# Optimization experiments

Measured on AMD Instinct MI355X. Metric: run time of the kernel, lower is better.

## Reference

```python
import jax, jax.numpy as jnp
import numpy as np

N = 50000
E = 800000
FEAT = 128
COND = 64
HID = 128
LAT = 64


def setup_inputs() -> dict:
    key = jax.random.key(0)
    ks = jax.random.split(key, 16)
    inp = {
        "feature": jax.random.normal(ks[0], (N, FEAT), jnp.float32),
        "condition": jax.random.normal(ks[1], (N, COND), jnp.float32),
        "edge_index": jax.random.randint(ks[2], (2, E), 0, N, jnp.int64 if jax.config.jax_enable_x64 else jnp.int32),
        "noise": jax.random.normal(ks[3], (N, LAT), jnp.float32),
        # GCNConv params (glorot-style scale)
        "W_f2h": jax.random.normal(ks[4], (FEAT, HID), jnp.float32) * (1.0 / np.sqrt(FEAT)),
        "b_f2h": jnp.zeros((HID,), jnp.float32),
        "W_c2h": jax.random.normal(ks[5], (COND, HID), jnp.float32) * (1.0 / np.sqrt(COND)),
        "b_c2h": jnp.zeros((HID,), jnp.float32),
        "W_h2h": jax.random.normal(ks[6], (2 * HID, HID), jnp.float32) * (1.0 / np.sqrt(2 * HID)),
        "b_h2h": jnp.zeros((HID,), jnp.float32),
        "W_mean": jax.random.normal(ks[7], (HID, LAT), jnp.float32) * (1.0 / np.sqrt(HID)),
        "b_mean": jnp.zeros((LAT,), jnp.float32),
        "W_logvar": jax.random.normal(ks[8], (HID, LAT), jnp.float32) * (1.0 / np.sqrt(HID)),
        "b_logvar": jnp.zeros((LAT,), jnp.float32),
    }
    return inp


def _gcn_norm(edge_index, n):
    # add self-loops, compute symmetric normalization deg^-1/2 * deg^-1/2
    loop = jnp.arange(n, dtype=edge_index.dtype)
    src = jnp.concatenate([edge_index[0], loop])
    dst = jnp.concatenate([edge_index[1], loop])
    deg = jax.ops.segment_sum(jnp.ones_like(src, jnp.float32), dst, num_segments=n)
    dinv = jnp.where(deg > 0, jax.lax.rsqrt(deg), 0.0)
    norm = dinv[src] * dinv[dst]  # [E+N]
    return src, dst, norm


def _gcn_conv(x, W, b, src, dst, norm, n):
    h = x @ W                                  # [N, out]
    msg = h[src] * norm[:, None]               # gather + scale, [E+N, out]
    out = jax.ops.segment_sum(msg, dst, num_segments=n)
    return out + b


def reference(feature, condition, edge_index, noise,
              W_f2h, b_f2h, W_c2h, b_c2h, W_h2h, b_h2h,
              W_mean, b_mean, W_logvar, b_logvar):
    n = feature.shape[0]
    src, dst, norm = _gcn_norm(edge_index, n)
    f2h = jnp.tanh(_gcn_conv(feature, W_f2h, b_f2h, src, dst, norm, n))
    c2h = jnp.tanh(_gcn_conv(condition, W_c2h, b_c2h, src, dst, norm, n))
    h = jnp.concatenate([f2h, c2h], axis=1)
    h = jnp.tanh(_gcn_conv(h, W_h2h, b_h2h, src, dst, norm, n))
    mean = _gcn_conv(h, W_mean, b_mean, src, dst, norm, n)
    logvar = _gcn_conv(h, W_logvar, b_logvar, src, dst, norm, n)
    z = noise * jnp.exp(0.5 * logvar) + mean
    return (z, mean, logvar)
```

## Files before the change

### kernel.cpp

```cpp
#include <hip/hip_runtime.h>
#include <math.h>

namespace {

constexpr int N = 50000;
constexpr int E = 800000;

typedef __attribute__((ext_vector_type(8))) short short8;
typedef __attribute__((ext_vector_type(4))) float f32x4;
typedef __attribute__((ext_vector_type(2))) float f32x2;


__device__ inline unsigned short f2bf(float f) {
  unsigned int b = __float_as_uint(f);
  unsigned int r = (b + 0x7fffu + ((b >> 16) & 1u)) >> 16;
  return (unsigned short)r;
}
__device__ inline unsigned int pack2(float a, float b) {
  return (unsigned int)f2bf(a) | ((unsigned int)f2bf(b) << 16);
}


__device__ inline unsigned int pack4_fp8(float a, float b, float c, float d) {
  int w = 0;
  w = __builtin_amdgcn_cvt_pk_fp8_f32(a, b, w, false);
  w = __builtin_amdgcn_cvt_pk_fp8_f32(c, d, w, true);
  return (unsigned int)w;
}
__device__ inline unsigned char f2fp8(float v) {
  return (unsigned char)(__builtin_amdgcn_cvt_pk_fp8_f32(v, v, 0, false) & 0xff);
}


__global__ void zero_int(int* p, int n) {
  int i = blockIdx.x * blockDim.x + threadIdx.x;
  if (i < n) p[i] = 0;
}

__global__ __launch_bounds__(256) void count_xcd(const int* __restrict__ dst,
                                                 int* __restrict__ cnt) {
  constexpr int RANGE = (N + 7) / 8;
  int r = blockIdx.x & 7;
  int lo = r * RANGE;
  int hi = lo + RANGE;
  int nb = gridDim.x >> 3;
  int bi = blockIdx.x >> 3;
  for (int e = bi * 256 + threadIdx.x; e < E; e += nb * 256) {
    int d = dst[e];
    if (d >= lo && d < hi) atomicAdd(&cnt[d], 1);
  }
}

__global__ void block_sums(const int* __restrict__ cnt, int* __restrict__ bsum, int n) {
  int tid = threadIdx.x;
  int i = blockIdx.x * 256 + tid;
  int v = (i < n) ? cnt[i] : 0;
  for (int off = 32; off > 0; off >>= 1) v += __shfl_down(v, off, 64);
  __shared__ int sred[4];
  if ((tid & 63) == 0) sred[tid >> 6] = v;
  __syncthreads();
  if (tid == 0) bsum[blockIdx.x] = sred[0] + sred[1] + sred[2] + sred[3];
}

__global__ void scan_chunks2(const int* __restrict__ cnt, const int* __restrict__ bsum,
                             int nbk, int* __restrict__ row_ptr, int* __restrict__ cursor,
                             float* __restrict__ dinv, int n) {
  __shared__ int s[256];
  __shared__ int sred[4];
  __shared__ int sprefix;
  int tid = threadIdx.x;
  int pv = (tid < nbk && tid < (int)blockIdx.x) ? bsum[tid] : 0;
  for (int off = 32; off > 0; off >>= 1) pv += __shfl_down(pv, off, 64);
  if ((tid & 63) == 0) sred[tid >> 6] = pv;
  __syncthreads();
  if (tid == 0) sprefix = sred[0] + sred[1] + sred[2] + sred[3];
  int i = blockIdx.x * 256 + tid;
  int v = (i < n) ? cnt[i] : 0;
  s[tid] = v;
  __syncthreads();
  for (int d = 1; d < 256; d <<= 1) {
    int t = (tid >= d) ? s[tid - d] : 0;
    __syncthreads();
    s[tid] += t;
    __syncthreads();
  }
  if (i < n) {
    int excl = sprefix + s[tid] - v;
    row_ptr[i] = excl;
    cursor[i] = excl;
    dinv[i] = rsqrtf((float)(v + 1));
    if (i == n - 1) row_ptr[n] = excl + v;
  }
}

__global__ __launch_bounds__(256) void scatter_xcd(const int* __restrict__ src,
                                                   const int* __restrict__ dst,
                                                   int* __restrict__ cursor,
                                                   int* __restrict__ csr_src) {
  constexpr int RANGE = (N + 7) / 8;
  int r = blockIdx.x & 7;
  int lo = r * RANGE;
  int hi = lo + RANGE;
  int nb = gridDim.x >> 3;
  int bi = blockIdx.x >> 3;
  for (int e = bi * 256 + threadIdx.x; e < E; e += nb * 256) {
    int d = dst[e];
    if (d >= lo && d < hi) {
      int pos = atomicAdd(&cursor[d], 1);
      csr_src[pos] = src[e];
    }
  }
}


__global__ void cvt_cond(const float* __restrict__ in, const float* __restrict__ dinv,
                         unsigned char* __restrict__ out, int n) {
  int t = blockIdx.x * blockDim.x + threadIdx.x;
  if (t >= n * 8) return;
  int i = t >> 3, j = t & 7;
  float di = dinv[i];
  const float* s = in + (size_t)i * 64 + j * 8;
  float4 a = *(const float4*)s;
  float4 b = *(const float4*)(s + 4);
  uint2 o;
  o.x = pack4_fp8(di * a.x, di * a.y, di * a.z, di * a.w);
  o.y = pack4_fp8(di * b.x, di * b.y, di * b.z, di * b.w);
  *(uint2*)(out + (size_t)i * 192 + 128 + j * 8) = o;
}

__global__ void pack_w(const float* __restrict__ W1, int s1,
                       const float* __restrict__ W2, int s2, int split,
                       int ksteps, unsigned short* __restrict__ out) {
  int t = blockIdx.x * blockDim.x + threadIdx.x;
  int total = ksteps * 8 * 64;
  if (t >= total) return;
  int ks = t >> 9;
  int ct = (t >> 6) & 7;
  int l = t & 63;
  int k0 = ks * 32 + ((l >> 4) << 3);
  int col = ct * 16 + (l & 15);
  const float* src;
  int c;
  if (col < split) { src = W1 + col; c = s1; }
  else { src = W2 + (col - split); c = s2; }
  unsigned short* o = out + (size_t)t * 8;
#pragma unroll
  for (int i = 0; i < 8; ++i) o[i] = f2bf(src[(size_t)(k0 + i) * c]);
}

__global__ void make_bcat(const float* __restrict__ bm, const float* __restrict__ bl,
                          float* __restrict__ bcat) {
  int j = threadIdx.x;
  if (j < 64) bcat[j] = bm[j];
  else if (j < 128) bcat[j] = bl[j - 64];
}


template <int K, int EPI, bool F32A, int OUT>
__global__ __launch_bounds__(256) void gemm_mfma(const void* __restrict__ Av, int lda,
                                                 const unsigned short* __restrict__ Wp,
                                                 const float* __restrict__ bias_or_scale,
                                                 void* __restrict__ Cv, int ldc, int n) {
  constexpr int KSTEPS = K / 32;
  int tid = threadIdx.x;
  int w = tid >> 6;
  int l = tid & 63;
  int r0 = blockIdx.x * 128 + w * 32;
  int arow = l & 15;
  int kgrp = l >> 4;

  f32x4 acc[2][8];
#pragma unroll
  for (int m = 0; m < 2; ++m)
#pragma unroll
    for (int ct = 0; ct < 8; ++ct) acc[m][ct] = (f32x4)(0.f);

  int ra0 = min(r0 + arow, n - 1);
  int ra1 = min(r0 + 16 + arow, n - 1);

#pragma unroll 1
  for (int ks = 0; ks < KSTEPS; ++ks) {
    short8 a0, a1;
    if (F32A) {
      const float* p0 = (const float*)Av + (size_t)ra0 * lda + kgrp * 8 + ks * 32;
      const float* p1 = (const float*)Av + (size_t)ra1 * lda + kgrp * 8 + ks * 32;
      float4 x0 = *(const float4*)p0, y0 = *(const float4*)(p0 + 4);
      float4 x1 = *(const float4*)p1, y1 = *(const float4*)(p1 + 4);
      unsigned int u[4];
      u[0] = pack2(x0.x, x0.y); u[1] = pack2(x0.z, x0.w);
      u[2] = pack2(y0.x, y0.y); u[3] = pack2(y0.z, y0.w);
      a0 = *(const short8*)u;
      u[0] = pack2(x1.x, x1.y); u[1] = pack2(x1.z, x1.w);
      u[2] = pack2(y1.x, y1.y); u[3] = pack2(y1.z, y1.w);
      a1 = *(const short8*)u;
    } else {
      a0 = *(const short8*)((const unsigned short*)Av + (size_t)ra0 * lda + kgrp * 8 + ks * 32);
      a1 = *(const short8*)((const unsigned short*)Av + (size_t)ra1 * lda + kgrp * 8 + ks * 32);
    }
    const short8* pb = (const short8*)Wp + (size_t)(ks * 8) * 64 + l;
#pragma unroll
    for (int ct = 0; ct < 8; ++ct) {
      short8 b = pb[ct * 64];
      acc[0][ct] = __builtin_amdgcn_mfma_f32_16x16x32_bf16(a0, b, acc[0][ct], 0, 0, 0);
      acc[1][ct] = __builtin_amdgcn_mfma_f32_16x16x32_bf16(a1, b, acc[1][ct], 0, 0, 0);
    }
  }

  int ccol = l & 15;
  int crow = (l >> 4) * 4;
#pragma unroll
  for (int ct = 0; ct < 8; ++ct) {
    int col = ct * 16 + ccol;
    float bv = (EPI == 1) ? bias_or_scale[col] : 0.f;
#pragma unroll
    for (int m = 0; m < 2; ++m) {
#pragma unroll
      for (int r = 0; r < 4; ++r) {
        int row = r0 + m * 16 + crow + r;
        if (row < n) {
          float v = acc[m][ct][r];
          if (EPI == 1) v = tanhf(v + bv);
          if (EPI == 2) v = v * bias_or_scale[row];
          if (OUT == 0)
            ((unsigned short*)Cv)[(size_t)row * ldc + col] = f2bf(v);
          else
            ((unsigned char*)Cv)[(size_t)row * ldc + col] = f2fp8(v);
        }
      }
    }
  }
}


#define ACC16_ADD_FP8(ACC, U)                                           \
  {                                                                     \
    f32x2 t0 = __builtin_amdgcn_cvt_pk_f32_fp8((int)U.x, false);        \
    f32x2 t1 = __builtin_amdgcn_cvt_pk_f32_fp8((int)U.x, true);         \
    f32x2 t2 = __builtin_amdgcn_cvt_pk_f32_fp8((int)U.y, false);        \
    f32x2 t3 = __builtin_amdgcn_cvt_pk_f32_fp8((int)U.y, true);         \
    f32x2 t4 = __builtin_amdgcn_cvt_pk_f32_fp8((int)U.z, false);        \
    f32x2 t5 = __builtin_amdgcn_cvt_pk_f32_fp8((int)U.z, true);         \
    f32x2 t6 = __builtin_amdgcn_cvt_pk_f32_fp8((int)U.w, false);        \
    f32x2 t7 = __builtin_amdgcn_cvt_pk_f32_fp8((int)U.w, true);         \
    ACC[0] += t0[0]; ACC[1] += t0[1]; ACC[2] += t1[0]; ACC[3] += t1[1]; \
    ACC[4] += t2[0]; ACC[5] += t2[1]; ACC[6] += t3[0]; ACC[7] += t3[1]; \
    ACC[8] += t4[0]; ACC[9] += t4[1]; ACC[10] += t5[0]; ACC[11] += t5[1]; \
    ACC[12] += t6[0]; ACC[13] += t6[1]; ACC[14] += t7[0]; ACC[15] += t7[1]; \
  }

#define EDGE_WALK_PIPE(LANES, ROWSTRIDE)                                \
  int deg = e1 - e0;                                                    \
  int idxA = csr_src[e0 + wl];                                          \
  int idxB = csr_src[e0 + LANES + wl];                                  \
  int cnext = e0 + 2 * LANES;                                           \
  int t = 0;                                                            \
  while (t < deg) {                                                     \
    int idxN = csr_src[cnext + wl];                                     \
    _Pragma("unroll")                                                   \
    for (int k = 0; k < LANES; ++k) {                                   \
      if (t + k < deg) {                                                \
        int s = __shfl(idxA, rowbase + k);                              \
        uint4 u = X16[(size_t)s * ROWSTRIDE + wl];                      \
        ACC16_ADD_FP8(acc, u)                                           \
      }                                                                 \
    }                                                                   \
    idxA = idxB; idxB = idxN;                                           \
    cnext += LANES; t += LANES;                                         \
  }


__global__ __launch_bounds__(256) void prop192(const unsigned char* __restrict__ X,
                                               unsigned short* __restrict__ f2h_out,
                                               unsigned short* __restrict__ pc_out,
                                               const int* __restrict__ row_ptr,
                                               const int* __restrict__ csr_src,
                                               const float* __restrict__ dinv,
                                               const float* __restrict__ b_f2h, int n) {
  int wave = threadIdx.x >> 6;
  int wlane = threadIdx.x & 63;
  int rrow = wlane / 12;
  int wl = wlane - rrow * 12;
  if (rrow >= 5) return;
  int rowbase = rrow * 12;
  int i = blockIdx.x * 20 + wave * 5 + rrow;
  if (i >= n) return;
  const uint4* X16 = (const uint4*)X;
  float di = dinv[i];
  float acc[16];
#pragma unroll
  for (int j = 0; j < 16; ++j) acc[j] = 0.f;
  {
    uint4 u = X16[(size_t)i * 12 + wl];
    ACC16_ADD_FP8(acc, u)
  }
  int e0 = row_ptr[i], e1 = row_ptr[i + 1];
  EDGE_WALK_PIPE(12, 12)

  if (wl < 8) {
    float out[16];
#pragma unroll
    for (int j = 0; j < 16; ++j) out[j] = tanhf(fmaf(di, acc[j], b_f2h[wl * 16 + j]));
    unsigned short* yp = f2h_out + (size_t)i * 256 + wl * 16;
    uint4 o0, o1;
    o0.x = pack2(out[0], out[1]); o0.y = pack2(out[2], out[3]);
    o0.z = pack2(out[4], out[5]); o0.w = pack2(out[6], out[7]);
    o1.x = pack2(out[8], out[9]); o1.y = pack2(out[10], out[11]);
    o1.z = pack2(out[12], out[13]); o1.w = pack2(out[14], out[15]);
    *(uint4*)yp = o0;
    *(uint4*)(yp + 8) = o1;
  } else {
    unsigned short* yp = pc_out + (size_t)i * 64 + (wl - 8) * 16;
    uint4 o0, o1;
    o0.x = pack2(di * acc[0], di * acc[1]); o0.y = pack2(di * acc[2], di * acc[3]);
    o0.z = pack2(di * acc[4], di * acc[5]); o0.w = pack2(di * acc[6], di * acc[7]);
    o1.x = pack2(di * acc[8], di * acc[9]); o1.y = pack2(di * acc[10], di * acc[11]);
    o1.z = pack2(di * acc[12], di * acc[13]); o1.w = pack2(di * acc[14], di * acc[15]);
    *(uint4*)yp = o0;
    *(uint4*)(yp + 8) = o1;
  }
}


__global__ __launch_bounds__(256) void prop128(const unsigned char* __restrict__ X,
                                               unsigned short* __restrict__ Y,
                                               const int* __restrict__ row_ptr,
                                               const int* __restrict__ csr_src,
                                               const float* __restrict__ dinv,
                                               const float* __restrict__ bias, int n) {
  int wl = threadIdx.x & 7;
  int rloc = threadIdx.x >> 3;
  int rowbase = (threadIdx.x & 63) & ~7;
  int i = blockIdx.x * 32 + rloc;
  if (i >= n) return;
  const uint4* X16 = (const uint4*)X;
  float di = dinv[i];
  float acc[16];
#pragma unroll
  for (int j = 0; j < 16; ++j) acc[j] = 0.f;
  {
    uint4 u = X16[(size_t)i * 8 + wl];
    ACC16_ADD_FP8(acc, u)
  }
  int e0 = row_ptr[i], e1 = row_ptr[i + 1];
  EDGE_WALK_PIPE(8, 8)

  float out[16];
#pragma unroll
  for (int j = 0; j < 16; ++j) out[j] = tanhf(fmaf(di, acc[j], bias[wl * 16 + j]));
  unsigned short* yp = Y + (size_t)i * 128 + wl * 16;
  uint4 o0, o1;
  o0.x = pack2(out[0], out[1]); o0.y = pack2(out[2], out[3]);
  o0.z = pack2(out[4], out[5]); o0.w = pack2(out[6], out[7]);
  o1.x = pack2(out[8], out[9]); o1.y = pack2(out[10], out[11]);
  o1.z = pack2(out[12], out[13]); o1.w = pack2(out[14], out[15]);
  *(uint4*)yp = o0;
  *(uint4*)(yp + 8) = o1;
}


__global__ __launch_bounds__(256) void prop_fin(const unsigned char* __restrict__ X,
                                                const int* __restrict__ row_ptr,
                                                const int* __restrict__ csr_src,
                                                const float* __restrict__ dinv,
                                                const float* __restrict__ bcat,
                                                const float* __restrict__ noise,
                                                float* __restrict__ out, int n) {
  int wl = threadIdx.x & 7;
  int rloc = threadIdx.x >> 3;
  int rowbase = (threadIdx.x & 63) & ~7;
  int i = blockIdx.x * 32 + rloc;
  if (i >= n) return;
  const uint4* X16 = (const uint4*)X;
  float di = dinv[i];
  float acc[16];
#pragma unroll
  for (int j = 0; j < 16; ++j) acc[j] = 0.f;
  {
    uint4 u = X16[(size_t)i * 8 + wl];
    ACC16_ADD_FP8(acc, u)
  }
  int e0 = row_ptr[i], e1 = row_ptr[i + 1];
  EDGE_WALK_PIPE(8, 8)

  float v[16];
#pragma unroll
  for (int j = 0; j < 16; ++j) v[j] = fmaf(di, acc[j], bcat[wl * 16 + j]);
  const float* nz = noise + (size_t)i * 64 + (wl & 3) * 16;
  float tt[16];
#pragma unroll
  for (int j = 0; j < 16; ++j) tt[j] = nz[j] * expf(0.5f * v[j]);
  int srcl = rowbase + 4 + (wl & 3);
  float z[16];
#pragma unroll
  for (int j = 0; j < 16; ++j) z[j] = v[j] + __shfl(tt[j], srcl);

  size_t n64 = (size_t)n * 64;
  if (wl < 4) {
    float* zp = out + (size_t)i * 64 + wl * 16;
    *(float4*)zp = make_float4(z[0], z[1], z[2], z[3]);
    *(float4*)(zp + 4) = make_float4(z[4], z[5], z[6], z[7]);
    *(float4*)(zp + 8) = make_float4(z[8], z[9], z[10], z[11]);
    *(float4*)(zp + 12) = make_float4(z[12], z[13], z[14], z[15]);
    float* mp = out + n64 + (size_t)i * 64 + wl * 16;
    *(float4*)mp = make_float4(v[0], v[1], v[2], v[3]);
    *(float4*)(mp + 4) = make_float4(v[4], v[5], v[6], v[7]);
    *(float4*)(mp + 8) = make_float4(v[8], v[9], v[10], v[11]);
    *(float4*)(mp + 12) = make_float4(v[12], v[13], v[14], v[15]);
  } else {
    float* lp = out + 2 * n64 + (size_t)i * 64 + (wl - 4) * 16;
    *(float4*)lp = make_float4(v[0], v[1], v[2], v[3]);
    *(float4*)(lp + 4) = make_float4(v[4], v[5], v[6], v[7]);
    *(float4*)(lp + 8) = make_float4(v[8], v[9], v[10], v[11]);
    *(float4*)(lp + 12) = make_float4(v[12], v[13], v[14], v[15]);
  }
}

}

extern "C" void kernel_launch(void* const* d_in, const int* in_sizes, int n_in,
                              void* d_out, int out_size, void* d_ws, size_t ws_size,
                              hipStream_t stream) {
  const float* feature   = (const float*)d_in[0];
  const float* condition = (const float*)d_in[1];
  const int*   ei        = (const int*)d_in[2];
  const float* noise     = (const float*)d_in[3];
  const float* W_f2h     = (const float*)d_in[4];
  const float* b_f2h     = (const float*)d_in[5];
  const float* W_c2h     = (const float*)d_in[6];
  const float* b_c2h     = (const float*)d_in[7];
  const float* W_h2h     = (const float*)d_in[8];
  const float* b_h2h     = (const float*)d_in[9];
  const float* W_mean    = (const float*)d_in[10];
  const float* b_mean    = (const float*)d_in[11];
  const float* W_logvar  = (const float*)d_in[12];
  const float* b_logvar  = (const float*)d_in[13];

  const int* src = ei;
  const int* dst = ei + E;

  char* p = (char*)d_ws;
  auto alloc = [&](size_t bytes) {
    char* q = p;
    p += (bytes + 255) & ~(size_t)255;
    return q;
  };
  unsigned char*  buf192 = (unsigned char*)alloc((size_t)N * 192);
  unsigned char*  u2buf  = (unsigned char*)alloc((size_t)N * 128);
  unsigned char*  vbuf   = (unsigned char*)alloc((size_t)N * 128);
  unsigned short* catbuf = (unsigned short*)alloc((size_t)N * 256 * 2);
  unsigned short* Pcbf   = (unsigned short*)alloc((size_t)N * 64 * 2);
  unsigned short* hbuf   = (unsigned short*)alloc((size_t)N * 128 * 2);
  int*   cnt     = (int*)alloc((size_t)N * 4);
  int*   cursor  = (int*)alloc((size_t)N * 4);
  int*   row_ptr = (int*)alloc((size_t)(N + 1) * 4);
  int*   csr_src = (int*)alloc((size_t)E * 4 + 1024);
  int*   bsum    = (int*)alloc(256 * 4);
  float* dinv    = (float*)alloc((size_t)N * 4);
  unsigned short* Wf2h_p = (unsigned short*)alloc(4 * 512 * 8 * 2);
  unsigned short* Wc2h_p = (unsigned short*)alloc(2 * 512 * 8 * 2);
  unsigned short* Wh2h_p = (unsigned short*)alloc(8 * 512 * 8 * 2);
  unsigned short* Wcat_p = (unsigned short*)alloc(4 * 512 * 8 * 2);
  float* bcat    = (float*)alloc(128 * 4);
  (void)ws_size; (void)in_sizes; (void)n_in; (void)out_size;

  int nb = (N + 255) / 256;

  zero_int<<<nb, 256, 0, stream>>>(cnt, N);
  count_xcd<<<1024, 256, 0, stream>>>(dst, cnt);
  block_sums<<<nb, 256, 0, stream>>>(cnt, bsum, N);
  scan_chunks2<<<nb, 256, 0, stream>>>(cnt, bsum, nb, row_ptr, cursor, dinv, N);
  scatter_xcd<<<1024, 256, 0, stream>>>(src, dst, cursor, csr_src);

  cvt_cond<<<(N * 8 + 255) / 256, 256, 0, stream>>>(condition, dinv, buf192, N);
  pack_w<<<(4 * 512 + 255) / 256, 256, 0, stream>>>(W_f2h, 128, nullptr, 0, 128, 4, Wf2h_p);
  pack_w<<<(2 * 512 + 255) / 256, 256, 0, stream>>>(W_c2h, 128, nullptr, 0, 128, 2, Wc2h_p);
  pack_w<<<(8 * 512 + 255) / 256, 256, 0, stream>>>(W_h2h, 128, nullptr, 0, 128, 8, Wh2h_p);
  pack_w<<<(4 * 512 + 255) / 256, 256, 0, stream>>>(W_mean, 64, W_logvar, 64, 64, 4, Wcat_p);
  make_bcat<<<1, 128, 0, stream>>>(b_mean, b_logvar, bcat);

  int ggrid = (N + 127) / 128;

  gemm_mfma<128, 2, true, 1><<<ggrid, 256, 0, stream>>>(feature, 128, Wf2h_p, dinv, buf192, 192, N);
  prop192<<<(N + 19) / 20, 256, 0, stream>>>(buf192, catbuf, Pcbf, row_ptr, csr_src, dinv, b_f2h, N);
  gemm_mfma<64, 1, false, 0><<<ggrid, 256, 0, stream>>>(Pcbf, 64, Wc2h_p, b_c2h, catbuf + 128, 256, N);
  gemm_mfma<256, 2, false, 1><<<ggrid, 256, 0, stream>>>(catbuf, 256, Wh2h_p, dinv, u2buf, 128, N);
  prop128<<<(N + 31) / 32, 256, 0, stream>>>(u2buf, hbuf, row_ptr, csr_src, dinv, b_h2h, N);
  gemm_mfma<128, 2, false, 1><<<ggrid, 256, 0, stream>>>(hbuf, 128, Wcat_p, dinv, vbuf, 128, N);
  prop_fin<<<(N + 31) / 32, 256, 0, stream>>>(vbuf, row_ptr, csr_src, dinv, bcat, noise,
                                              (float*)d_out, N);
}
```

Baseline: 269.6 us.

## Split propagation kernels into 64-column phases to shrink gather working set

Each sparse propagation kernel is split into several launches that each handle one 64-byte FP8 column slice, with 4 lanes per row instead of 8 or 12. The aim is to keep each pass's gathered slice of the node feature table resident in cache, improving hit rates on random row gathers. The cost is re-reading the CSR index arrays once per phase, extra kernel launches, and a temporary float buffer that carries the noise*exp term from the logvar pass to the mean pass.

After: 316.6 us. 1.17x slower.

```diff
diff --git a/kernel.cpp b/kernel.cpp
--- a/kernel.cpp
+++ b/kernel.cpp
@@ -248,171 +248,157 @@
     ACC[12] += t6[0]; ACC[13] += t6[1]; ACC[14] += t7[0]; ACC[15] += t7[1]; \
   }
 
-#define EDGE_WALK_PIPE(LANES, ROWSTRIDE)                                \
+#define EDGE_WALK_P4(XB, RSTRIDE)                                       \
   int deg = e1 - e0;                                                    \
   int idxA = csr_src[e0 + wl];                                          \
-  int idxB = csr_src[e0 + LANES + wl];                                  \
-  int cnext = e0 + 2 * LANES;                                           \
+  int idxB = csr_src[e0 + 4 + wl];                                      \
+  int cnext = e0 + 8;                                                   \
   int t = 0;                                                            \
   while (t < deg) {                                                     \
     int idxN = csr_src[cnext + wl];                                     \
     _Pragma("unroll")                                                   \
-    for (int k = 0; k < LANES; ++k) {                                   \
+    for (int k = 0; k < 4; ++k) {                                       \
       if (t + k < deg) {                                                \
         int s = __shfl(idxA, rowbase + k);                              \
-        uint4 u = X16[(size_t)s * ROWSTRIDE + wl];                      \
+        uint4 u = XB[(size_t)s * RSTRIDE + wl];                         \
         ACC16_ADD_FP8(acc, u)                                           \
       }                                                                 \
     }                                                                   \
     idxA = idxB; idxB = idxN;                                           \
-    cnext += LANES; t += LANES;                                         \
-  }
-
-
-__global__ __launch_bounds__(256) void prop192(const unsigned char* __restrict__ X,
-                                               unsigned short* __restrict__ f2h_out,
-                                               unsigned short* __restrict__ pc_out,
-                                               const int* __restrict__ row_ptr,
-                                               const int* __restrict__ csr_src,
-                                               const float* __restrict__ dinv,
-                                               const float* __restrict__ b_f2h, int n) {
-  int wave = threadIdx.x >> 6;
-  int wlane = threadIdx.x & 63;
-  int rrow = wlane / 12;
-  int wl = wlane - rrow * 12;
-  if (rrow >= 5) return;
-  int rowbase = rrow * 12;
-  int i = blockIdx.x * 20 + wave * 5 + rrow;
-  if (i >= n) return;
-  const uint4* X16 = (const uint4*)X;
-  float di = dinv[i];
-  float acc[16];
-#pragma unroll
-  for (int j = 0; j < 16; ++j) acc[j] = 0.f;
-  {
-    uint4 u = X16[(size_t)i * 12 + wl];
-    ACC16_ADD_FP8(acc, u)
-  }
-  int e0 = row_ptr[i], e1 = row_ptr[i + 1];
-  EDGE_WALK_PIPE(12, 12)
-
-  if (wl < 8) {
-    float out[16];
-#pragma unroll
-    for (int j = 0; j < 16; ++j) out[j] = tanhf(fmaf(di, acc[j], b_f2h[wl * 16 + j]));
-    unsigned short* yp = f2h_out + (size_t)i * 256 + wl * 16;
-    uint4 o0, o1;
-    o0.x = pack2(out[0], out[1]); o0.y = pack2(out[2], out[3]);
-    o0.z = pack2(out[4], out[5]); o0.w = pack2(out[6], out[7]);
-    o1.x = pack2(out[8], out[9]); o1.y = pack2(out[10], out[11]);
-    o1.z = pack2(out[12], out[13]); o1.w = pack2(out[14], out[15]);
-    *(uint4*)yp = o0;
-    *(uint4*)(yp + 8) = o1;
-  } else {
-    unsigned short* yp = pc_out + (size_t)i * 64 + (wl - 8) * 16;
-    uint4 o0, o1;
-    o0.x = pack2(di * acc[0], di * acc[1]); o0.y = pack2(di * acc[2], di * acc[3]);
-    o0.z = pack2(di * acc[4], di * acc[5]); o0.w = pack2(di * acc[6], di * acc[7]);
-    o1.x = pack2(di * acc[8], di * acc[9]); o1.y = pack2(di * acc[10], di * acc[11]);
-    o1.z = pack2(di * acc[12], di * acc[13]); o1.w = pack2(di * acc[14], di * acc[15]);
-    *(uint4*)yp = o0;
-    *(uint4*)(yp + 8) = o1;
-  }
-}
-
-
-__global__ __launch_bounds__(256) void prop128(const unsigned char* __restrict__ X,
-                                               unsigned short* __restrict__ Y,
+    cnext += 4; t += 4;                                                 \
+  }
+
+
+template <int RSTRIDE, int PHOFF, int EPI>
+__global__ __launch_bounds__(256) void prop_ph(const unsigned char* __restrict__ X,
+                                               unsigned short* __restrict__ Y, int ldy,
+                                               int col0,
                                                const int* __restrict__ row_ptr,
                                                const int* __restrict__ csr_src,
                                                const float* __restrict__ dinv,
                                                const float* __restrict__ bias, int n) {
-  int wl = threadIdx.x & 7;
-  int rloc = threadIdx.x >> 3;
-  int rowbase = (threadIdx.x & 63) & ~7;
-  int i = blockIdx.x * 32 + rloc;
+  int wl = threadIdx.x & 3;
+  int rloc = threadIdx.x >> 2;
+  int rowbase = (threadIdx.x & 63) & ~3;
+  int i = blockIdx.x * 64 + rloc;
   if (i >= n) return;
-  const uint4* X16 = (const uint4*)X;
+  const uint4* XB = (const uint4*)X + PHOFF;
   float di = dinv[i];
   float acc[16];
 #pragma unroll
   for (int j = 0; j < 16; ++j) acc[j] = 0.f;
   {
-    uint4 u = X16[(size_t)i * 8 + wl];
+    uint4 u = XB[(size_t)i * RSTRIDE + wl];
     ACC16_ADD_FP8(acc, u)
   }
   int e0 = row_ptr[i], e1 = row_ptr[i + 1];
-  EDGE_WALK_PIPE(8, 8)
-
-  float out[16];
-#pragma unroll
-  for (int j = 0; j < 16; ++j) out[j] = tanhf(fmaf(di, acc[j], bias[wl * 16 + j]));
-  unsigned short* yp = Y + (size_t)i * 128 + wl * 16;
+  EDGE_WALK_P4(XB, RSTRIDE)
+
+  float o[16];
+  if (EPI == 0) {
+#pragma unroll
+    for (int j = 0; j < 16; ++j) o[j] = tanhf(fmaf(di, acc[j], bias[col0 + wl * 16 + j]));
+  } else {
+#pragma unroll
+    for (int j = 0; j < 16; ++j) o[j] = di * acc[j];
+  }
+  unsigned short* yp = Y + (size_t)i * ldy + col0 + wl * 16;
   uint4 o0, o1;
-  o0.x = pack2(out[0], out[1]); o0.y = pack2(out[2], out[3]);
-  o0.z = pack2(out[4], out[5]); o0.w = pack2(out[6], out[7]);
-  o1.x = pack2(out[8], out[9]); o1.y = pack2(out[10], out[11]);
-  o1.z = pack2(out[12], out[13]); o1.w = pack2(out[14], out[15]);
+  o0.x = pack2(o[0], o[1]); o0.y = pack2(o[2], o[3]);
+  o0.z = pack2(o[4], o[5]); o0.w = pack2(o[6], o[7]);
+  o1.x = pack2(o[8], o[9]); o1.y = pack2(o[10], o[11]);
+  o1.z = pack2(o[12], o[13]); o1.w = pack2(o[14], o[15]);
   *(uint4*)yp = o0;
   *(uint4*)(yp + 8) = o1;
 }
 
 
-__global__ __launch_bounds__(256) void prop_fin(const unsigned char* __restrict__ X,
-                                                const int* __restrict__ row_ptr,
-                                                const int* __restrict__ csr_src,
-                                                const float* __restrict__ dinv,
-                                                const float* __restrict__ bcat,
-                                                const float* __restrict__ noise,
-                                                float* __restrict__ out, int n) {
-  int wl = threadIdx.x & 7;
-  int rloc = threadIdx.x >> 3;
-  int rowbase = (threadIdx.x & 63) & ~7;
-  int i = blockIdx.x * 32 + rloc;
+__global__ __launch_bounds__(256) void prop_fin_lv(const unsigned char* __restrict__ X,
+                                                   const int* __restrict__ row_ptr,
+                                                   const int* __restrict__ csr_src,
+                                                   const float* __restrict__ dinv,
+                                                   const float* __restrict__ bcat,
+                                                   const float* __restrict__ noise,
+                                                   float* __restrict__ out,
+                                                   float* __restrict__ tbuf, int n) {
+  int wl = threadIdx.x & 3;
+  int rloc = threadIdx.x >> 2;
+  int rowbase = (threadIdx.x & 63) & ~3;
+  int i = blockIdx.x * 64 + rloc;
   if (i >= n) return;
-  const uint4* X16 = (const uint4*)X;
+  const uint4* XB = (const uint4*)X + 4;
   float di = dinv[i];
   float acc[16];
 #pragma unroll
   for (int j = 0; j < 16; ++j) acc[j] = 0.f;
   {
-    uint4 u = X16[(size_t)i * 8 + wl];
+    uint4 u = XB[(size_t)i * 8 + wl];
     ACC16_ADD_FP8(acc, u)
   }
   int e0 = row_ptr[i], e1 = row_ptr[i + 1];
-  EDGE_WALK_PIPE(8, 8)
-
-  float v[16];
-#pragma unroll
-  for (int j = 0; j < 16; ++j) v[j] = fmaf(di, acc[j], bcat[wl * 16 + j]);
-  const float* nz = noise + (size_t)i * 64 + (wl & 3) * 16;
-  float tt[16];
-#pragma unroll
-  for (int j = 0; j < 16; ++j) tt[j] = nz[j] * expf(0.5f * v[j]);
-  int srcl = rowbase + 4 + (wl & 3);
-  float z[16];
-#pragma unroll
-  for (int j = 0; j < 16; ++j) z[j] = v[j] + __shfl(tt[j], srcl);
-
-  size_t n64 = (size_t)n * 64;
-  if (wl < 4) {
-    float* zp = out + (size_t)i * 64 + wl * 16;
-    *(float4*)zp = make_float4(z[0], z[1], z[2], z[3]);
-    *(float4*)(zp + 4) = make_float4(z[4], z[5], z[6], z[7]);
-    *(float4*)(zp + 8) = make_float4(z[8], z[9], z[10], z[11]);
-    *(float4*)(zp + 12) = make_float4(z[12], z[13], z[14], z[15]);
-    float* mp = out + n64 + (size_t)i * 64 + wl * 16;
-    *(float4*)mp = make_float4(v[0], v[1], v[2], v[3]);
-    *(float4*)(mp + 4) = make_float4(v[4], v[5], v[6], v[7]);
-    *(float4*)(mp + 8) = make_float4(v[8], v[9], v[10], v[11]);
-    *(float4*)(mp + 12) = make_float4(v[12], v[13], v[14], v[15]);
-  } else {
-    float* lp = out + 2 * n64 + (size_t)i * 64 + (wl - 4) * 16;
-    *(float4*)lp = make_float4(v[0], v[1], v[2], v[3]);
-    *(float4*)(lp + 4) = make_float4(v[4], v[5], v[6], v[7]);
-    *(float4*)(lp + 8) = make_float4(v[8], v[9], v[10], v[11]);
-    *(float4*)(lp + 12) = make_float4(v[12], v[13], v[14], v[15]);
-  }
+  EDGE_WALK_P4(XB, 8)
+
+  const float* nz = noise + (size_t)i * 64 + wl * 16;
+  float lv[16], tt[16];
+#pragma unroll
+  for (int j = 0; j < 16; ++j) {
+    lv[j] = fmaf(di, acc[j], bcat[64 + wl * 16 + j]);
+    tt[j] = nz[j] * expf(0.5f * lv[j]);
+  }
+  float* lp = out + (size_t)2 * n * 64 + (size_t)i * 64 + wl * 16;
+  *(float4*)lp = make_float4(lv[0], lv[1], lv[2], lv[3]);
+  *(float4*)(lp + 4) = make_float4(lv[4], lv[5], lv[6], lv[7]);
+  *(float4*)(lp + 8) = make_float4(lv[8], lv[9], lv[10], lv[11]);
+  *(float4*)(lp + 12) = make_float4(lv[12], lv[13], lv[14], lv[15]);
+  float* tp = tbuf + (size_t)i * 64 + wl * 16;
+  *(float4*)tp = make_float4(tt[0], tt[1], tt[2], tt[3]);
+  *(float4*)(tp + 4) = make_float4(tt[4], tt[5], tt[6], tt[7]);
+  *(float4*)(tp + 8) = make_float4(tt[8], tt[9], tt[10], tt[11]);
+  *(float4*)(tp + 12) = make_float4(tt[12], tt[13], tt[14], tt[15]);
+}
+
+
+__global__ __launch_bounds__(256) void prop_fin_mean(const unsigned char* __restrict__ X,
+                                                     const int* __restrict__ row_ptr,
+                                                     const int* __restrict__ csr_src,
+                                                     const float* __restrict__ dinv,
+                                                     const float* __restrict__ bcat,
+                                                     const float* __restrict__ tbuf,
+                                                     float* __restrict__ out, int n) {
+  int wl = threadIdx.x & 3;
+  int rloc = threadIdx.x >> 2;
+  int rowbase = (threadIdx.x & 63) & ~3;
+  int i = blockIdx.x * 64 + rloc;
+  if (i >= n) return;
+  const uint4* XB = (const uint4*)X;
+  float di = dinv[i];
+  float acc[16];
+#pragma unroll
+  for (int j = 0; j < 16; ++j) acc[j] = 0.f;
+  {
+    uint4 u = XB[(size_t)i * 8 + wl];
+    ACC16_ADD_FP8(acc, u)
+  }
+  int e0 = row_ptr[i], e1 = row_ptr[i + 1];
+  EDGE_WALK_P4(XB, 8)
+
+  const float* tp = tbuf + (size_t)i * 64 + wl * 16;
+  float mv[16], z[16];
+#pragma unroll
+  for (int j = 0; j < 16; ++j) {
+    mv[j] = fmaf(di, acc[j], bcat[wl * 16 + j]);
+    z[j] = mv[j] + tp[j];
+  }
+  float* zp = out + (size_t)i * 64 + wl * 16;
+  *(float4*)zp = make_float4(z[0], z[1], z[2], z[3]);
+  *(float4*)(zp + 4) = make_float4(z[4], z[5], z[6], z[7]);
+  *(float4*)(zp + 8) = make_float4(z[8], z[9], z[10], z[11]);
+  *(float4*)(zp + 12) = make_float4(z[12], z[13], z[14], z[15]);
+  float* mp = out + (size_t)n * 64 + (size_t)i * 64 + wl * 16;
+  *(float4*)mp = make_float4(mv[0], mv[1], mv[2], mv[3]);
+  *(float4*)(mp + 4) = make_float4(mv[4], mv[5], mv[6], mv[7]);
+  *(float4*)(mp + 8) = make_float4(mv[8], mv[9], mv[10], mv[11]);
+  *(float4*)(mp + 12) = make_float4(mv[12], mv[13], mv[14], mv[15]);
 }
 
 }
@@ -450,6 +436,7 @@
   unsigned short* catbuf = (unsigned short*)alloc((size_t)N * 256 * 2);
   unsigned short* Pcbf   = (unsigned short*)alloc((size_t)N * 64 * 2);
   unsigned short* hbuf   = (unsigned short*)alloc((size_t)N * 128 * 2);
+  float*          tbuf   = (float*)alloc((size_t)N * 64 * 4);
   int*   cnt     = (int*)alloc((size_t)N * 4);
   int*   cursor  = (int*)alloc((size_t)N * 4);
   int*   row_ptr = (int*)alloc((size_t)(N + 1) * 4);
@@ -479,13 +466,19 @@
   make_bcat<<<1, 128, 0, stream>>>(b_mean, b_logvar, bcat);
 
   int ggrid = (N + 127) / 128;
+  int pgrid = (N + 63) / 64;
 
   gemm_mfma<128, 2, true, 1><<<ggrid, 256, 0, stream>>>(feature, 128, Wf2h_p, dinv, buf192, 192, N);
-  prop192<<<(N + 19) / 20, 256, 0, stream>>>(buf192, catbuf, Pcbf, row_ptr, csr_src, dinv, b_f2h, N);
+  prop_ph<12, 0, 0><<<pgrid, 256, 0, stream>>>(buf192, catbuf, 256, 0, row_ptr, csr_src, dinv, b_f2h, N);
+  prop_ph<12, 4, 0><<<pgrid, 256, 0, stream>>>(buf192, catbuf, 256, 64, row_ptr, csr_src, dinv, b_f2h, N);
+  prop_ph<12, 8, 1><<<pgrid, 256, 0, stream>>>(buf192, Pcbf, 64, 0, row_ptr, csr_src, dinv, nullptr, N);
   gemm_mfma<64, 1, false, 0><<<ggrid, 256, 0, stream>>>(Pcbf, 64, Wc2h_p, b_c2h, catbuf + 128, 256, N);
   gemm_mfma<256, 2, false, 1><<<ggrid, 256, 0, stream>>>(catbuf, 256, Wh2h_p, dinv, u2buf, 128, N);
-  prop128<<<(N + 31) / 32, 256, 0, stream>>>(u2buf, hbuf, row_ptr, csr_src, dinv, b_h2h, N);
+  prop_ph<8, 0, 0><<<pgrid, 256, 0, stream>>>(u2buf, hbuf, 128, 0, row_ptr, csr_src, dinv, b_h2h, N);
+  prop_ph<8, 4, 0><<<pgrid, 256, 0, stream>>>(u2buf, hbuf, 128, 64, row_ptr, csr_src, dinv, b_h2h, N);
   gemm_mfma<128, 2, false, 1><<<ggrid, 256, 0, stream>>>(hbuf, 128, Wcat_p, dinv, vbuf, 128, N);
-  prop_fin<<<(N + 31) / 32, 256, 0, stream>>>(vbuf, row_ptr, csr_src, dinv, bcat, noise,
-                                              (float*)d_out, N);
-}
+  prop_fin_lv<<<pgrid, 256, 0, stream>>>(vbuf, row_ptr, csr_src, dinv, bcat, noise,
+                                         (float*)d_out, tbuf, N);
+  prop_fin_mean<<<pgrid, 256, 0, stream>>>(vbuf, row_ptr, csr_src, dinv, bcat, tbuf,
+                                           (float*)d_out, N);
+}
```
